# Performance work log

Hardware: AMD Instinct MI355X
Metric: run time of the kernel (lower is better)

## Reference

```python
import jax, jax.numpy as jnp
import numpy as np

N_HEADS = 8  # from init_kwargs


def setup_inputs() -> dict:
    key = jax.random.key(0)
    ks = jax.random.split(key, 12)
    P, B, V, F = 12, 32, 32, 256          # len_pred, batch, n_vehicles, feature_size
    S, NL, LF = 32, 16, 64                # lane_size, n_lanes, lane_feature_size
    T = 20                                # obs horizon for mask_input
    inp = {
        "query": jax.random.normal(ks[0], (P, B, V, F), jnp.float32),
        "lanes": jax.random.normal(ks[1], (S, B, NL, LF), jnp.float32),
        "mask_input": jax.random.bernoulli(ks[2], 0.8, (T, B, V)),
        "mask_lanes": jax.random.bernoulli(ks[3], 0.8, (S, B, NL)),
        # nn.Linear params stored as (in, out) so y = x @ W + b
        "Wk": jax.random.normal(ks[4], (LF, F), jnp.float32) * 0.05,
        "bk": jax.random.normal(ks[5], (F,), jnp.float32) * 0.05,
        "Wv": jax.random.normal(ks[6], (LF, F), jnp.float32) * 0.05,
        "bv": jax.random.normal(ks[7], (F,), jnp.float32) * 0.05,
        "Wc": jax.random.normal(ks[8], (F, F), jnp.float32) * 0.05,
        "bc": jax.random.normal(ks[9], (F,), jnp.float32) * 0.05,
    }
    return inp


def reference(query, lanes, mask_input, mask_lanes, Wk, bk, Wv, bv, Wc, bc):
    P, B, V, F = query.shape
    S, _, NL, LF = lanes.shape
    H = N_HEADS
    d = F // H
    L = NL * S

    # lanes: (S,B,NL,LF) -> (B, NL*S, LF)  [lane-major flatten, as in torch]
    lanes_f = lanes.transpose(1, 2, 0, 3).reshape(B, L, LF)
    key = (lanes_f @ Wk + bk).reshape(B, L, H, d).transpose(0, 2, 1, 3)    # (B,H,L,d)
    value = (lanes_f @ Wv + bv).reshape(B, L, H, d).transpose(0, 2, 1, 3)  # (B,H,L,d)

    # mask_lanes: (S,B,NL) -> (B, S*NL)  [position-major flatten, as in torch]
    ml = mask_lanes[:S].transpose(1, 0, 2).reshape(B, S * NL)
    mi = jnp.any(mask_input, axis=0)              # (B,V): valid at any obs step
    mask = ml[:, None, :] & mi[:, :, None]        # (B,V,L)

    q = query.reshape(P, B, V, H, d).transpose(0, 1, 3, 2, 4)  # (P,B,H,V,d)

    # scale=1 in the original call -> no 1/sqrt(d_k) division
    scores = jnp.einsum('pbhvd,bhld->pbhvl', q, key)           # (P,B,H,V,L)
    scores = jnp.where(mask[None, :, None, :, :], scores, -1e9)
    p_attn = jax.nn.softmax(scores, axis=-1)

    # geometric aggregation: exp(P @ log(sigmoid(V)))
    out = jnp.exp(jnp.einsum('pbhvl,bhld->pbhvd', p_attn, jax.nn.log_sigmoid(value)))
    out = out.transpose(0, 1, 3, 2, 4).reshape(P, B, V, F)
    return out @ Wc + bc  # attention_combine (n_heads > 1)
```

## Files before the change

### kernel.cpp

```cpp
#include <hip/hip_runtime.h>
#include <cstdint>

#define P_ 12
#define B_ 32
#define V_ 32
#define F_ 256
#define S_ 32
#define NL_ 16
#define LF_ 64
#define T_ 20
#define H_ 8
#define D_ 32
#define L_ 512

typedef short bf16x8 __attribute__((ext_vector_type(8)));
typedef short bf16x4 __attribute__((ext_vector_type(4)));
typedef float f32x4 __attribute__((ext_vector_type(4)));

static __device__ __forceinline__ short f2bf(float f) {
  uint32_t u = __builtin_bit_cast(uint32_t, f);
  uint32_t r = u + 0x7FFFu + ((u >> 16) & 1u);
  return (short)(r >> 16);
}

static __device__ __forceinline__ uint32_t cvtpk(float lo, float hi) {
  uint32_t r;
  asm("v_cvt_pk_bf16_f32 %0, %1, %2" : "=v"(r) : "v"(lo), "v"(hi));
  return r;
}
static __device__ __forceinline__ bf16x8 pack8(uint32_t d0, uint32_t d1,
                                               uint32_t d2, uint32_t d3) {
  uint4 u = {d0, d1, d2, d3};
  return __builtin_bit_cast(bf16x8, u);
}
static __device__ __forceinline__ bf16x4 pack4(uint32_t d0, uint32_t d1) {
  uint2 u = {d0, d1};
  return __builtin_bit_cast(bf16x4, u);
}

__global__ __launch_bounds__(256) void prep_kernel(
    const float* __restrict__ Wk, const float* __restrict__ Wv,
    const float* __restrict__ Wc,
    const int* __restrict__ mask_input, const int* __restrict__ mask_lanes,
    short* __restrict__ WkT, short* __restrict__ WvT, short* __restrict__ WcT,
    unsigned int* __restrict__ maskr, int* __restrict__ mi) {
  int t = blockIdx.x * 256 + threadIdx.x;
  if (t < 2048) {
    int f = t >> 3, k0 = (t & 7) * 8;
    bf16x8 o;
#pragma unroll
    for (int e = 0; e < 8; ++e) o[e] = f2bf(Wk[(k0 + e) * F_ + f]);
    *(bf16x8*)&WkT[f * LF_ + k0] = o;
  } else if (t < 4096) {
    int i = t - 2048;
    int f = i >> 3, k0 = (i & 7) * 8;
    bf16x8 o;
#pragma unroll
    for (int e = 0; e < 8; ++e) o[e] = f2bf(Wv[(k0 + e) * F_ + f]);
    *(bf16x8*)&WvT[f * LF_ + k0] = o;
  } else if (t < 12288) {
    int i = t - 4096;
    int f = i >> 5, k0 = (i & 31) * 8;
    bf16x8 o;
#pragma unroll
    for (int e = 0; e < 8; ++e) o[e] = f2bf(Wc[(k0 + e) * F_ + f]);
    *(bf16x8*)&WcT[f * F_ + k0] = o;
  } else if (t < 12800) {
    int i = t - 12288;
    int b = i >> 4, r = i & 15;
    unsigned int bits = 0u;
    for (int lt = 0; lt < 32; ++lt)
      if (mask_lanes[(lt * B_ + b) * NL_ + r]) bits |= (1u << lt);
    maskr[i] = bits;
  } else if (t < 13824) {
    int i = t - 12800;
    int b = i >> 5, v = i & 31;
    int any = 0;
    for (int tt = 0; tt < T_; ++tt) any |= mask_input[(tt * B_ + b) * V_ + v];
    mi[i] = any ? 1 : 0;
  }
}

__global__ __launch_bounds__(512, 2) void attn_kernel(
    const float* __restrict__ query, const float* __restrict__ lanes,
    const short* __restrict__ WkT, const short* __restrict__ WvT,
    const float* __restrict__ bk, const float* __restrict__ bv,
    const unsigned int* __restrict__ maskr, const int* __restrict__ mi,
    short* __restrict__ out0b) {
  __shared__ short Ks[512 * 40];
  __shared__ short Vt[32 * 520];

  int i0 = blockIdx.x;
  int xcd = i0 & 7, sl0 = i0 >> 3;
  int b = xcd * 4 + (sl0 >> 3), h = sl0 & 7;

  int tid = threadIdx.x;
  int w = tid >> 6, lane = tid & 63;
  int r = lane & 15, g = lane >> 4;
  const f32x4 zero = {0.f, 0.f, 0.f, 0.f};

  {
    bf16x8 wk[2][2], wv[2][2];
#pragma unroll
    for (int dt = 0; dt < 2; ++dt)
#pragma unroll
      for (int c = 0; c < 2; ++c) {
        int f = h * 32 + dt * 16 + r;
        wk[dt][c] = *(const bf16x8*)&WkT[f * LF_ + c * 32 + g * 8];
        wv[dt][c] = *(const bf16x8*)&WvT[f * LF_ + c * 32 + g * 8];
      }
    float4 bk4[2];
    float bvf[2];
#pragma unroll
    for (int dt = 0; dt < 2; ++dt) {
      bk4[dt] = *(const float4*)&bk[h * 32 + dt * 16 + g * 4];
      bvf[dt] = bv[h * 32 + dt * 16 + r];
    }

#pragma unroll
    for (int lt = 0; lt < 4; ++lt) {
      int l0 = w * 64 + lt * 16;
      int l = l0 + r;
      int nl = l >> 5, s = l & 31;
      const float* xrow = &lanes[((s * B_ + b) * NL_ + nl) * LF_];
      bf16x8 xf[2];
#pragma unroll
      for (int c = 0; c < 2; ++c) {
        float4 a = *(const float4*)&xrow[c * 32 + g * 8];
        float4 q = *(const float4*)&xrow[c * 32 + g * 8 + 4];
        xf[c] = pack8(cvtpk(a.x, a.y), cvtpk(a.z, a.w),
                      cvtpk(q.x, q.y), cvtpk(q.z, q.w));
      }
      int sl = (l & ~31) | (((l >> 2) & 1) << 4) | (((l >> 3) & 3) << 2) | (l & 3);
#pragma unroll
      for (int dt = 0; dt < 2; ++dt) {
        f32x4 aK = __builtin_amdgcn_mfma_f32_16x16x32_bf16(wk[dt][0], xf[0], zero, 0, 0, 0);
        aK = __builtin_amdgcn_mfma_f32_16x16x32_bf16(wk[dt][1], xf[1], aK, 0, 0, 0);
        *(bf16x4*)&Ks[sl * 40 + dt * 16 + g * 4] =
            pack4(cvtpk(aK[0] + bk4[dt].x, aK[1] + bk4[dt].y),
                  cvtpk(aK[2] + bk4[dt].z, aK[3] + bk4[dt].w));
        f32x4 aV = __builtin_amdgcn_mfma_f32_16x16x32_bf16(xf[0], wv[dt][0], zero, 0, 0, 0);
        aV = __builtin_amdgcn_mfma_f32_16x16x32_bf16(xf[1], wv[dt][1], aV, 0, 0, 0);
        float ls[4];
#pragma unroll
        for (int reg = 0; reg < 4; ++reg) {
          float x = aV[reg] + bvf[dt];
          ls[reg] = fminf(x, 0.f) - log1pf(__expf(-fabsf(x)));
        }
        *(bf16x4*)&Vt[(dt * 16 + r) * 520 + l0 + g * 4] =
            pack4(cvtpk(ls[0], ls[1]), cvtpk(ls[2], ls[3]));
      }
    }
  }

  bf16x8 qf[3];
  float mivf[3];
#pragma unroll
  for (int bi = 0; bi < 3; ++bi) {
    int band = w + bi * 8;
    int p = band >> 1, vb = (band & 1) << 4;
    const float* qp = &query[((p * B_ + b) * V_ + vb + r) * F_ + h * D_ + g * 8];
    float4 a = *(const float4*)qp;
    float4 q = *(const float4*)(qp + 4);
    qf[bi] = pack8(cvtpk(a.x, a.y), cvtpk(a.z, a.w),
                   cvtpk(q.x, q.y), cvtpk(q.z, q.w));
    mivf[bi] = mi[b * V_ + vb + r] ? 1.f : 0.f;
  }
  unsigned int mw[8];
#pragma unroll
  for (int q8 = 0; q8 < 8; ++q8) mw[q8] = maskr[b * 16 + ((g & 1) << 3) + q8];
  int ghalf = g >> 1;

  float rsum[3] = {0.f, 0.f, 0.f};
  f32x4 O[3][2];
#pragma unroll
  for (int bi = 0; bi < 3; ++bi) { O[bi][0] = zero; O[bi][1] = zero; }

  __syncthreads();

  for (int ch = 0; ch < 4; ++ch) {
    bf16x8 Kf[8];
#pragma unroll
    for (int t = 0; t < 8; ++t)
      Kf[t] = *(const bf16x8*)&Ks[((ch * 8 + t) * 16 + r) * 40 + g * 8];

    bf16x8 vbuf[4][2];
#pragma unroll
    for (int ks = 0; ks < 4; ++ks) {
      vbuf[ks][0] = *(const bf16x8*)&Vt[r * 520 + ch * 128 + ks * 32 + g * 8];
      vbuf[ks][1] = *(const bf16x8*)&Vt[(16 + r) * 520 + ch * 128 + ks * 32 + g * 8];
    }

    float fb[8][4];
#pragma unroll
    for (int t = 0; t < 8; ++t) {
      int bitidx = ch * 8 + 2 * (t >> 1) + ghalf;
#pragma unroll
      for (int j = 0; j < 4; ++j)
        fb[t][j] = ((mw[4 * (t & 1) + j] >> bitidx) & 1u) ? -40.f : -1e9f;
    }

#pragma unroll
    for (int bi = 0; bi < 3; ++bi) {
      f32x4 sc[8];
#pragma unroll
      for (int t = 0; t < 8; ++t)
        sc[t] = __builtin_amdgcn_mfma_f32_16x16x32_bf16(Kf[t], qf[bi], zero, 0, 0, 0);
      float pp[8][4];
#pragma unroll
      for (int t = 0; t < 8; ++t)
#pragma unroll
        for (int j = 0; j < 4; ++j) {
          float p = __expf(sc[t][j] + fb[t][j]) * mivf[bi];
          pp[t][j] = p;
          rsum[bi] += p;
        }
#pragma unroll
      for (int ks = 0; ks < 4; ++ks) {
        bf16x8 pa = pack8(cvtpk(pp[2 * ks][0], pp[2 * ks][1]),
                          cvtpk(pp[2 * ks][2], pp[2 * ks][3]),
                          cvtpk(pp[2 * ks + 1][0], pp[2 * ks + 1][1]),
                          cvtpk(pp[2 * ks + 1][2], pp[2 * ks + 1][3]));
        O[bi][0] = __builtin_amdgcn_mfma_f32_16x16x32_bf16(pa, vbuf[ks][0], O[bi][0], 0, 0, 0);
        O[bi][1] = __builtin_amdgcn_mfma_f32_16x16x32_bf16(pa, vbuf[ks][1], O[bi][1], 0, 0, 0);
      }
    }
  }

#pragma unroll
  for (int bi = 0; bi < 3; ++bi) {
    int band = w + bi * 8;
    int p = band >> 1, vb = (band & 1) << 4;
    float rs = rsum[bi];
    rs += __shfl_xor(rs, 16);
    rs += __shfl_xor(rs, 32);
    float invv = rs > 0.f ? 1.f / rs : 0.f;
#pragma unroll
    for (int j = 0; j < 4; ++j) {
      float inv = __shfl(invv, g * 4 + j);
      int v = vb + g * 4 + j;
      short* op = &out0b[((p * B_ + b) * V_ + v) * F_ + h * D_];
      op[r] = f2bf(__expf(O[bi][0][j] * inv));
      op[16 + r] = f2bf(__expf(O[bi][1][j] * inv));
    }
  }
}

__global__ __launch_bounds__(256) void combine_kernel(
    const short* __restrict__ out0b, const short* __restrict__ WcT,
    const float* __restrict__ bc, float* __restrict__ out) {
  int tid = threadIdx.x;
  int w = tid >> 6, lane = tid & 63;
  int r = lane & 15, g = lane >> 4;
  int R = blockIdx.x * 64 + w * 16;

  bf16x8 xf[8];
#pragma unroll
  for (int c = 0; c < 8; ++c)
    xf[c] = *(const bf16x8*)&out0b[(R + r) * F_ + c * 32 + g * 8];

  const f32x4 zero = {0.f, 0.f, 0.f, 0.f};
#pragma unroll 2
  for (int ft = 0; ft < 16; ++ft) {
    f32x4 acc = zero;
#pragma unroll
    for (int c = 0; c < 8; ++c) {
      bf16x8 wf = *(const bf16x8*)&WcT[(ft * 16 + r) * F_ + c * 32 + g * 8];
      acc = __builtin_amdgcn_mfma_f32_16x16x32_bf16(wf, xf[c], acc, 0, 0, 0);
    }
    float4 bc4 = *(const float4*)&bc[ft * 16 + g * 4];
    float4 o;
    o.x = acc[0] + bc4.x;
    o.y = acc[1] + bc4.y;
    o.z = acc[2] + bc4.z;
    o.w = acc[3] + bc4.w;
    *(float4*)&out[(R + r) * F_ + ft * 16 + g * 4] = o;
  }
}

extern "C" void kernel_launch(void* const* d_in, const int* in_sizes, int n_in,
                              void* d_out, int out_size, void* d_ws, size_t ws_size,
                              hipStream_t stream) {
  const float* query = (const float*)d_in[0];
  const float* lanes = (const float*)d_in[1];
  const int* mask_input = (const int*)d_in[2];
  const int* mask_lanes = (const int*)d_in[3];
  const float* Wk = (const float*)d_in[4];
  const float* bk = (const float*)d_in[5];
  const float* Wv = (const float*)d_in[6];
  const float* bv = (const float*)d_in[7];
  const float* Wc = (const float*)d_in[8];
  const float* bc = (const float*)d_in[9];
  float* out = (float*)d_out;

  char* wp = (char*)d_ws;
  short* out0b = (short*)wp; wp += 6291456;
  short* WkT = (short*)wp;   wp += 32768;
  short* WvT = (short*)wp;   wp += 32768;
  short* WcT = (short*)wp;   wp += 131072;
  unsigned int* maskr = (unsigned int*)wp; wp += 2048;
  int* mi = (int*)wp;        wp += 4096;

  prep_kernel<<<54, 256, 0, stream>>>(Wk, Wv, Wc, mask_input, mask_lanes,
                                      WkT, WvT, WcT, maskr, mi);
  attn_kernel<<<B_ * H_, 512, 0, stream>>>(query, lanes, WkT, WvT, bk, bv,
                                           maskr, mi, out0b);
  combine_kernel<<<P_ * B_ * V_ / 64, 256, 0, stream>>>(out0b, WcT, bc, out);
}
```

Baseline: 60.51 us.

## Split attention blocks three ways over prediction bands and store head-major intermediate

The attention grid triples so that each block handles one third of the query bands (one band per wave instead of three), which raises block count and occupancy across the 256 CUs. Every block now recomputes the K/V projection and log-sigmoid for its (b,h), so that projection work triples. The intermediate output is rewritten in a head-major layout, which makes each 32-element head row contiguous for the attention store, and the combine kernel's loads are adjusted to match.

```diff
diff --git a/kernel.cpp b/kernel.cpp
--- a/kernel.cpp
+++ b/kernel.cpp
@@ -91,8 +91,10 @@
   __shared__ short Vt[32 * 520];
 
   int i0 = blockIdx.x;
-  int xcd = i0 & 7, sl0 = i0 >> 3;
-  int b = xcd * 4 + (sl0 >> 3), h = sl0 & 7;
+  int xcd = i0 & 7, widx = i0 >> 3;
+  int b = xcd * 4 + widx / 24;
+  int rem = widx % 24;
+  int h = rem & 7, pg = rem >> 3;
 
   int tid = threadIdx.x;
   int w = tid >> 6, lane = tid & 63;
@@ -153,28 +155,22 @@
     }
   }
 
-  bf16x8 qf[3];
-  float mivf[3];
-#pragma unroll
-  for (int bi = 0; bi < 3; ++bi) {
-    int band = w + bi * 8;
-    int p = band >> 1, vb = (band & 1) << 4;
-    const float* qp = &query[((p * B_ + b) * V_ + vb + r) * F_ + h * D_ + g * 8];
-    float4 a = *(const float4*)qp;
-    float4 q = *(const float4*)(qp + 4);
-    qf[bi] = pack8(cvtpk(a.x, a.y), cvtpk(a.z, a.w),
-                   cvtpk(q.x, q.y), cvtpk(q.z, q.w));
-    mivf[bi] = mi[b * V_ + vb + r] ? 1.f : 0.f;
-  }
+  int band = pg * 8 + w;
+  int p = band >> 1, vb = (band & 1) << 4;
+  const float* qp = &query[((p * B_ + b) * V_ + vb + r) * F_ + h * D_ + g * 8];
+  float4 qa = *(const float4*)qp;
+  float4 qq = *(const float4*)(qp + 4);
+  bf16x8 qf = pack8(cvtpk(qa.x, qa.y), cvtpk(qa.z, qa.w),
+                    cvtpk(qq.x, qq.y), cvtpk(qq.z, qq.w));
+  float mivf = mi[b * V_ + vb + r] ? 1.f : 0.f;
+
   unsigned int mw[8];
 #pragma unroll
   for (int q8 = 0; q8 < 8; ++q8) mw[q8] = maskr[b * 16 + ((g & 1) << 3) + q8];
   int ghalf = g >> 1;
 
-  float rsum[3] = {0.f, 0.f, 0.f};
-  f32x4 O[3][2];
-#pragma unroll
-  for (int bi = 0; bi < 3; ++bi) { O[bi][0] = zero; O[bi][1] = zero; }
+  float rsum = 0.f;
+  f32x4 O0 = zero, O1 = zero;
 
   __syncthreads();
 
@@ -191,58 +187,49 @@
       vbuf[ks][1] = *(const bf16x8*)&Vt[(16 + r) * 520 + ch * 128 + ks * 32 + g * 8];
     }
 
-    float fb[8][4];
-#pragma unroll
-    for (int t = 0; t < 8; ++t) {
-      int bitidx = ch * 8 + 2 * (t >> 1) + ghalf;
-#pragma unroll
-      for (int j = 0; j < 4; ++j)
-        fb[t][j] = ((mw[4 * (t & 1) + j] >> bitidx) & 1u) ? -40.f : -1e9f;
-    }
-
-#pragma unroll
-    for (int bi = 0; bi < 3; ++bi) {
-      f32x4 sc[8];
-#pragma unroll
-      for (int t = 0; t < 8; ++t)
-        sc[t] = __builtin_amdgcn_mfma_f32_16x16x32_bf16(Kf[t], qf[bi], zero, 0, 0, 0);
-      float pp[8][4];
-#pragma unroll
-      for (int t = 0; t < 8; ++t)
-#pragma unroll
-        for (int j = 0; j < 4; ++j) {
-          float p = __expf(sc[t][j] + fb[t][j]) * mivf[bi];
-          pp[t][j] = p;
-          rsum[bi] += p;
-        }
-#pragma unroll
-      for (int ks = 0; ks < 4; ++ks) {
-        bf16x8 pa = pack8(cvtpk(pp[2 * ks][0], pp[2 * ks][1]),
-                          cvtpk(pp[2 * ks][2], pp[2 * ks][3]),
-                          cvtpk(pp[2 * ks + 1][0], pp[2 * ks + 1][1]),
-                          cvtpk(pp[2 * ks + 1][2], pp[2 * ks + 1][3]));
-        O[bi][0] = __builtin_amdgcn_mfma_f32_16x16x32_bf16(pa, vbuf[ks][0], O[bi][0], 0, 0, 0);
-        O[bi][1] = __builtin_amdgcn_mfma_f32_16x16x32_bf16(pa, vbuf[ks][1], O[bi][1], 0, 0, 0);
-      }
-    }
-  }
-
-#pragma unroll
-  for (int bi = 0; bi < 3; ++bi) {
-    int band = w + bi * 8;
-    int p = band >> 1, vb = (band & 1) << 4;
-    float rs = rsum[bi];
-    rs += __shfl_xor(rs, 16);
-    rs += __shfl_xor(rs, 32);
-    float invv = rs > 0.f ? 1.f / rs : 0.f;
-#pragma unroll
-    for (int j = 0; j < 4; ++j) {
-      float inv = __shfl(invv, g * 4 + j);
-      int v = vb + g * 4 + j;
-      short* op = &out0b[((p * B_ + b) * V_ + v) * F_ + h * D_];
-      op[r] = f2bf(__expf(O[bi][0][j] * inv));
-      op[16 + r] = f2bf(__expf(O[bi][1][j] * inv));
-    }
+    f32x4 sc[8];
+#pragma unroll
+    for (int t = 0; t < 8; ++t)
+      sc[t] = __builtin_amdgcn_mfma_f32_16x16x32_bf16(Kf[t], qf, zero, 0, 0, 0);
+
+#pragma unroll
+    for (int ks = 0; ks < 4; ++ks) {
+      int bitidx = ch * 8 + 2 * ks + ghalf;
+      float f0 = ((mw[0] >> bitidx) & 1u) ? -40.f : -1e9f;
+      float f1 = ((mw[1] >> bitidx) & 1u) ? -40.f : -1e9f;
+      float f2 = ((mw[2] >> bitidx) & 1u) ? -40.f : -1e9f;
+      float f3 = ((mw[3] >> bitidx) & 1u) ? -40.f : -1e9f;
+      float f4 = ((mw[4] >> bitidx) & 1u) ? -40.f : -1e9f;
+      float f5 = ((mw[5] >> bitidx) & 1u) ? -40.f : -1e9f;
+      float f6 = ((mw[6] >> bitidx) & 1u) ? -40.f : -1e9f;
+      float f7 = ((mw[7] >> bitidx) & 1u) ? -40.f : -1e9f;
+      float p0 = __expf(sc[2 * ks][0] + f0) * mivf;
+      float p1 = __expf(sc[2 * ks][1] + f1) * mivf;
+      float p2 = __expf(sc[2 * ks][2] + f2) * mivf;
+      float p3 = __expf(sc[2 * ks][3] + f3) * mivf;
+      float p4 = __expf(sc[2 * ks + 1][0] + f4) * mivf;
+      float p5 = __expf(sc[2 * ks + 1][1] + f5) * mivf;
+      float p6 = __expf(sc[2 * ks + 1][2] + f6) * mivf;
+      float p7 = __expf(sc[2 * ks + 1][3] + f7) * mivf;
+      rsum += ((p0 + p1) + (p2 + p3)) + ((p4 + p5) + (p6 + p7));
+      bf16x8 pa = pack8(cvtpk(p0, p1), cvtpk(p2, p3),
+                        cvtpk(p4, p5), cvtpk(p6, p7));
+      O0 = __builtin_amdgcn_mfma_f32_16x16x32_bf16(pa, vbuf[ks][0], O0, 0, 0, 0);
+      O1 = __builtin_amdgcn_mfma_f32_16x16x32_bf16(pa, vbuf[ks][1], O1, 0, 0, 0);
+    }
+  }
+
+  float rs = rsum;
+  rs += __shfl_xor(rs, 16);
+  rs += __shfl_xor(rs, 32);
+  float invv = rs > 0.f ? 1.f / rs : 0.f;
+#pragma unroll
+  for (int j = 0; j < 4; ++j) {
+    float inv = __shfl(invv, g * 4 + j);
+    int v = vb + g * 4 + j;
+    short* op = &out0b[(((h * P_ + p) * B_ + b) * V_ + v) * D_];
+    op[r] = f2bf(__expf(O0[j] * inv));
+    op[16 + r] = f2bf(__expf(O1[j] * inv));
   }
 }
 
@@ -257,7 +244,7 @@
   bf16x8 xf[8];
 #pragma unroll
   for (int c = 0; c < 8; ++c)
-    xf[c] = *(const bf16x8*)&out0b[(R + r) * F_ + c * 32 + g * 8];
+    xf[c] = *(const bf16x8*)&out0b[(c * (P_ * B_ * V_) + R + r) * D_ + g * 8];
 
   const f32x4 zero = {0.f, 0.f, 0.f, 0.f};
 #pragma unroll 2
@@ -303,7 +290,7 @@
 
   prep_kernel<<<54, 256, 0, stream>>>(Wk, Wv, Wc, mask_input, mask_lanes,
                                       WkT, WvT, WcT, maskr, mi);
-  attn_kernel<<<B_ * H_, 512, 0, stream>>>(query, lanes, WkT, WvT, bk, bv,
-                                           maskr, mi, out0b);
+  attn_kernel<<<B_ * H_ * 3, 512, 0, stream>>>(query, lanes, WkT, WvT, bk, bv,
+                                               maskr, mi, out0b);
   combine_kernel<<<P_ * B_ * V_ / 64, 256, 0, stream>>>(out0b, WcT, bc, out);
 }
```

After: 86.93 us. 43.7% more time.
